# Optimization experiments

Measured on AMD Instinct MI355X. Metric: run time of the kernel, lower is better.

The kernel has to match this reference:

```python
import jax, jax.numpy as jnp
import numpy as np


def setup_inputs() -> dict:
    key = jax.random.key(0)
    k1, k2 = jax.random.split(key)
    B, N, M, D = 8, 4096, 4096, 3
    return {
        "input": jax.random.normal(k1, (B, N, D), dtype=jnp.float32),
        "target": jax.random.normal(k2, (B, M, D), dtype=jnp.float32),
    }


def reference(input, target):
    x2 = jnp.sum(input * input, axis=-1)          # [B, N]
    y2 = jnp.sum(target * target, axis=-1)        # [B, M]
    xy = jnp.einsum("bnd,bmd->bnm", input, target)  # [B, N, M]
    sqdist = x2[:, :, None] + y2[:, None, :] - 2.0 * xy
    sqdist = jnp.maximum(sqdist, 0.0)  # clamp numerical negatives
    sqdist1 = jnp.min(sqdist, axis=2)  # nearest target for each input point [B, N]
    sqdist2 = jnp.min(sqdist, axis=1)  # nearest input for each target point [B, M]
    return jnp.mean(sqdist1) + jnp.mean(sqdist2)
```

## Files before the change

### kernel.cpp

```cpp
#include <hip/hip_runtime.h>
#include <math.h>

#define BATCH 8
#define NPTS  4096
#define TPB   256
#define NCC   4
#define CHUNK (NPTS / NCC)
#define ROWS  256
#define NRC   (NPTS / ROWS)

typedef __bf16 bf16x8 __attribute__((ext_vector_type(8)));
typedef float  f32x16 __attribute__((ext_vector_type(16)));

__global__ __launch_bounds__(TPB) void chamfer_mfma_kernel(
    const float* __restrict__ input,
    const float* __restrict__ target,
    float* __restrict__ part)
{
  const int dir = blockIdx.z, b = blockIdx.y;
  const int rc = blockIdx.x & (NRC - 1);
  const int cc = blockIdx.x >> 4;

  const float* __restrict__ qp = (dir ? target : input) + (size_t)b * NPTS * 3;
  const float* __restrict__ cp = (dir ? input  : target) + (size_t)b * NPTS * 3;

  __shared__ bf16x8 sB[2][CHUNK];
  __shared__ bf16x8 sA[2][ROWS];

  {
    const int c0 = cc * CHUNK + (int)threadIdx.x * 4;
    const float4* __restrict__ cv = (const float4*)(cp + 3 * c0);
    const float4 f0 = cv[0], f1 = cv[1], f2 = cv[2];
    float xs[4] = { f0.x, f0.w, f1.z, f2.y };
    float ys[4] = { f0.y, f1.x, f1.w, f2.z };
    float zs[4] = { f0.z, f1.y, f2.x, f2.w };
    #pragma unroll
    for (int j = 0; j < 4; ++j) {
      const float mx = -2.f * xs[j], my = -2.f * ys[j], mz = -2.f * zs[j];
      const __bf16 hx = (__bf16)mx, hy = (__bf16)my, hz = (__bf16)mz;
      const __bf16 lx = (__bf16)(mx - (float)hx);
      const __bf16 ly = (__bf16)(my - (float)hy);
      const __bf16 lz = (__bf16)(mz - (float)hz);
      const float y2 = fmaf(xs[j], xs[j], fmaf(ys[j], ys[j], zs[j] * zs[j]));
      const __bf16 h2 = (__bf16)y2, l2 = (__bf16)(y2 - (float)h2);
      const __bf16 z0 = (__bf16)0.f;
      bf16x8 v0, v1;
      v0[0]=hx; v0[1]=hy; v0[2]=hz; v0[3]=lx; v0[4]=ly; v0[5]=lz; v0[6]=z0; v0[7]=z0;
      v1[0]=hx; v1[1]=hy; v1[2]=hz; v1[3]=h2; v1[4]=l2; v1[5]=z0; v1[6]=z0; v1[7]=z0;
      sB[0][threadIdx.x * 4 + j] = v0;
      sB[1][threadIdx.x * 4 + j] = v1;
    }
  }
  float qx, qy, qz;
  {
    const int r = rc * ROWS + (int)threadIdx.x;
    qx = qp[3*r]; qy = qp[3*r+1]; qz = qp[3*r+2];
    const __bf16 hx = (__bf16)qx, hy = (__bf16)qy, hz = (__bf16)qz;
    const __bf16 lx = (__bf16)(qx - (float)hx);
    const __bf16 ly = (__bf16)(qy - (float)hy);
    const __bf16 lz = (__bf16)(qz - (float)hz);
    const __bf16 z0 = (__bf16)0.f, o1 = (__bf16)1.f;
    bf16x8 v0, v1;
    v0[0]=hx; v0[1]=hy; v0[2]=hz; v0[3]=hx; v0[4]=hy; v0[5]=hz; v0[6]=z0; v0[7]=z0;
    v1[0]=lx; v1[1]=ly; v1[2]=lz; v1[3]=o1; v1[4]=o1; v1[5]=z0; v1[6]=z0; v1[7]=z0;
    sA[0][threadIdx.x] = v0;
    sA[1][threadIdx.x] = v1;
  }
  __syncthreads();

  const int lane = (int)threadIdx.x & 63;
  const int wave = (int)threadIdx.x >> 6;
  const int half = lane >> 5;
  const int l31  = lane & 31;

  const bf16x8 a0 = sA[half][wave * 64 + l31];
  const bf16x8 a1 = sA[half][wave * 64 + 32 + l31];

  float rm0[16], rm1[16];
  #pragma unroll
  for (int i = 0; i < 16; ++i) { rm0[i] = 3.4e38f; rm1[i] = 3.4e38f; }

  f32x16 zacc;
  #pragma unroll
  for (int i = 0; i < 16; ++i) zacc[i] = 0.f;

  #pragma unroll
  for (int m = 0; m < CHUNK / 32; m += 2) {
    const bf16x8 bfA = sB[half][m * 32 + l31];
    const bf16x8 bfB = sB[half][m * 32 + 32 + l31];
    const f32x16 dA0 = __builtin_amdgcn_mfma_f32_32x32x16_bf16(a0, bfA, zacc, 0, 0, 0);
    const f32x16 dA1 = __builtin_amdgcn_mfma_f32_32x32x16_bf16(a1, bfA, zacc, 0, 0, 0);
    const f32x16 dB0 = __builtin_amdgcn_mfma_f32_32x32x16_bf16(a0, bfB, zacc, 0, 0, 0);
    const f32x16 dB1 = __builtin_amdgcn_mfma_f32_32x32x16_bf16(a1, bfB, zacc, 0, 0, 0);
    #pragma unroll
    for (int i = 0; i < 16; ++i) {
      rm0[i] = fminf(fminf(dA0[i], dB0[i]), rm0[i]);
      rm1[i] = fminf(fminf(dA1[i], dB1[i]), rm1[i]);
    }
  }

  __syncthreads();
  float* __restrict__ scr = (float*)sB;
  #pragma unroll
  for (int r = 0; r < 16; ++r) {
    const int row0 = wave * 64 + (r & 3) + 8 * (r >> 2) + 4 * half;
    const int sw   = ((row0 & 7) << 2);
    scr[row0 * 32 + (l31 ^ sw)]        = rm0[r];
    scr[(row0 + 32) * 32 + (l31 ^ sw)] = rm1[r];
  }
  __syncthreads();

  const int t = (int)threadIdx.x;
  const float4* __restrict__ rp = (const float4*)(scr + t * 32);
  float mn = 3.4e38f;
  #pragma unroll
  for (int k = 0; k < 8; ++k) {
    const float4 v = rp[k ^ (t & 7)];
    mn = fminf(mn, fminf(fminf(v.x, v.y), fminf(v.z, v.w)));
  }
  const float x2 = fmaf(qx, qx, fmaf(qy, qy, qz * qz));
  part[((size_t)(dir * BATCH + b) * NCC + cc) * NPTS + rc * ROWS + t] =
      fmaxf(mn + x2, 0.f);
}

__global__ __launch_bounds__(TPB) void chamfer_reduce_kernel(
    const float* __restrict__ part, float* __restrict__ out)
{
  const int i = (blockIdx.x * TPB + (int)threadIdx.x) * 4;
  const int g = i >> 12;
  const int q = i & (NPTS - 1);

  const float* __restrict__ p = part + ((size_t)g * NCC) * NPTS + q;
  float4 mn = *(const float4*)p;
  #pragma unroll
  for (int cc = 1; cc < NCC; ++cc) {
    const float4 v = *(const float4*)(p + (size_t)cc * NPTS);
    mn.x = fminf(mn.x, v.x); mn.y = fminf(mn.y, v.y);
    mn.z = fminf(mn.z, v.z); mn.w = fminf(mn.w, v.w);
  }
  float s = mn.x + mn.y + mn.z + mn.w;
  #pragma unroll
  for (int off = 32; off > 0; off >>= 1)
    s += __shfl_down(s, off, 64);

  __shared__ float wsum[TPB / 64];
  if ((threadIdx.x & 63) == 0) wsum[threadIdx.x >> 6] = s;
  __syncthreads();
  if (threadIdx.x == 0) {
    const float v = wsum[0] + wsum[1] + wsum[2] + wsum[3];
    atomicAdd(out, v * (1.0f / (float)(BATCH * NPTS)));
  }
}

extern "C" void kernel_launch(void* const* d_in, const int* in_sizes, int n_in,
                              void* d_out, int out_size, void* d_ws, size_t ws_size,
                              hipStream_t stream) {
  const float* input  = (const float*)d_in[0];
  const float* target = (const float*)d_in[1];
  float* out  = (float*)d_out;
  float* part = (float*)d_ws;

  hipMemsetAsync(out, 0, sizeof(float), stream);

  dim3 grid1(NRC * NCC, BATCH, 2);
  chamfer_mfma_kernel<<<grid1, dim3(TPB), 0, stream>>>(input, target, part);

  dim3 grid2((2 * BATCH * NPTS) / (TPB * 4));
  chamfer_reduce_kernel<<<grid2, dim3(TPB), 0, stream>>>(part, out);
}
```

Measured before the change: 73.80 us.

## Fuse min and reduction into one kernel with full candidate set per block

Each block now stages all 4096 candidate points into shared memory instead of a quarter. It computes the full row minimum directly and reduces to the output with an atomic, which removes the partials buffer and the second reduce kernel. The grid shrinks fourfold to one block per CU with larger LDS use. This reduces latency hiding and puts the longer staging phase on the critical path.

```diff
diff --git a/kernel.cpp b/kernel.cpp
--- a/kernel.cpp
+++ b/kernel.cpp
@@ -4,51 +4,53 @@
 #define BATCH 8
 #define NPTS  4096
 #define TPB   256
-#define NCC   4
-#define CHUNK (NPTS / NCC)
 #define ROWS  256
 #define NRC   (NPTS / ROWS)
+#define CPT   (NPTS / TPB)
 
 typedef __bf16 bf16x8 __attribute__((ext_vector_type(8)));
 typedef float  f32x16 __attribute__((ext_vector_type(16)));
 
-__global__ __launch_bounds__(TPB) void chamfer_mfma_kernel(
+__global__ __launch_bounds__(TPB, 1) void chamfer_fused_kernel(
     const float* __restrict__ input,
     const float* __restrict__ target,
-    float* __restrict__ part)
+    float* __restrict__ out)
 {
-  const int dir = blockIdx.z, b = blockIdx.y;
-  const int rc = blockIdx.x & (NRC - 1);
-  const int cc = blockIdx.x >> 4;
+  const int dir = blockIdx.z, b = blockIdx.y, rc = blockIdx.x;
 
   const float* __restrict__ qp = (dir ? target : input) + (size_t)b * NPTS * 3;
   const float* __restrict__ cp = (dir ? input  : target) + (size_t)b * NPTS * 3;
 
-  __shared__ bf16x8 sB[2][CHUNK];
+  __shared__ bf16x8 sB[2][NPTS];
   __shared__ bf16x8 sA[2][ROWS];
+  __shared__ float  wsum[TPB / 64];
 
   {
-    const int c0 = cc * CHUNK + (int)threadIdx.x * 4;
+    const int c0 = (int)threadIdx.x * CPT;
     const float4* __restrict__ cv = (const float4*)(cp + 3 * c0);
-    const float4 f0 = cv[0], f1 = cv[1], f2 = cv[2];
-    float xs[4] = { f0.x, f0.w, f1.z, f2.y };
-    float ys[4] = { f0.y, f1.x, f1.w, f2.z };
-    float zs[4] = { f0.z, f1.y, f2.x, f2.w };
+    float f[3 * CPT];
     #pragma unroll
-    for (int j = 0; j < 4; ++j) {
-      const float mx = -2.f * xs[j], my = -2.f * ys[j], mz = -2.f * zs[j];
+    for (int i = 0; i < (3 * CPT) / 4; ++i) {
+      const float4 t = cv[i];
+      f[4 * i + 0] = t.x; f[4 * i + 1] = t.y;
+      f[4 * i + 2] = t.z; f[4 * i + 3] = t.w;
+    }
+    #pragma unroll
+    for (int j = 0; j < CPT; ++j) {
+      const float x = f[3 * j], y = f[3 * j + 1], z = f[3 * j + 2];
+      const float mx = -2.f * x, my = -2.f * y, mz = -2.f * z;
       const __bf16 hx = (__bf16)mx, hy = (__bf16)my, hz = (__bf16)mz;
       const __bf16 lx = (__bf16)(mx - (float)hx);
       const __bf16 ly = (__bf16)(my - (float)hy);
       const __bf16 lz = (__bf16)(mz - (float)hz);
-      const float y2 = fmaf(xs[j], xs[j], fmaf(ys[j], ys[j], zs[j] * zs[j]));
+      const float y2 = fmaf(x, x, fmaf(y, y, z * z));
       const __bf16 h2 = (__bf16)y2, l2 = (__bf16)(y2 - (float)h2);
       const __bf16 z0 = (__bf16)0.f;
       bf16x8 v0, v1;
       v0[0]=hx; v0[1]=hy; v0[2]=hz; v0[3]=lx; v0[4]=ly; v0[5]=lz; v0[6]=z0; v0[7]=z0;
       v1[0]=hx; v1[1]=hy; v1[2]=hz; v1[3]=h2; v1[4]=l2; v1[5]=z0; v1[6]=z0; v1[7]=z0;
-      sB[0][threadIdx.x * 4 + j] = v0;
-      sB[1][threadIdx.x * 4 + j] = v1;
+      sB[0][c0 + j] = v0;
+      sB[1][c0 + j] = v1;
     }
   }
   float qx, qy, qz;
@@ -84,8 +86,8 @@
   #pragma unroll
   for (int i = 0; i < 16; ++i) zacc[i] = 0.f;
 
-  #pragma unroll
-  for (int m = 0; m < CHUNK / 32; m += 2) {
+  #pragma unroll 4
+  for (int m = 0; m < NPTS / 32; m += 2) {
     const bf16x8 bfA = sB[half][m * 32 + l31];
     const bf16x8 bfB = sB[half][m * 32 + 32 + l31];
     const f32x16 dA0 = __builtin_amdgcn_mfma_f32_32x32x16_bf16(a0, bfA, zacc, 0, 0, 0);
@@ -119,31 +121,11 @@
     mn = fminf(mn, fminf(fminf(v.x, v.y), fminf(v.z, v.w)));
   }
   const float x2 = fmaf(qx, qx, fmaf(qy, qy, qz * qz));
-  part[((size_t)(dir * BATCH + b) * NCC + cc) * NPTS + rc * ROWS + t] =
-      fmaxf(mn + x2, 0.f);
-}
+  float s = fmaxf(mn + x2, 0.f);
 
-__global__ __launch_bounds__(TPB) void chamfer_reduce_kernel(
-    const float* __restrict__ part, float* __restrict__ out)
-{
-  const int i = (blockIdx.x * TPB + (int)threadIdx.x) * 4;
-  const int g = i >> 12;
-  const int q = i & (NPTS - 1);
-
-  const float* __restrict__ p = part + ((size_t)g * NCC) * NPTS + q;
-  float4 mn = *(const float4*)p;
-  #pragma unroll
-  for (int cc = 1; cc < NCC; ++cc) {
-    const float4 v = *(const float4*)(p + (size_t)cc * NPTS);
-    mn.x = fminf(mn.x, v.x); mn.y = fminf(mn.y, v.y);
-    mn.z = fminf(mn.z, v.z); mn.w = fminf(mn.w, v.w);
-  }
-  float s = mn.x + mn.y + mn.z + mn.w;
   #pragma unroll
   for (int off = 32; off > 0; off >>= 1)
     s += __shfl_down(s, off, 64);
-
-  __shared__ float wsum[TPB / 64];
   if ((threadIdx.x & 63) == 0) wsum[threadIdx.x >> 6] = s;
   __syncthreads();
   if (threadIdx.x == 0) {
@@ -157,14 +139,11 @@
                               hipStream_t stream) {
   const float* input  = (const float*)d_in[0];
   const float* target = (const float*)d_in[1];
-  float* out  = (float*)d_out;
-  float* part = (float*)d_ws;
+  float* out = (float*)d_out;
+  (void)d_ws; (void)ws_size;
 
   hipMemsetAsync(out, 0, sizeof(float), stream);
 
-  dim3 grid1(NRC * NCC, BATCH, 2);
-  chamfer_mfma_kernel<<<grid1, dim3(TPB), 0, stream>>>(input, target, part);
-
-  dim3 grid2((2 * BATCH * NPTS) / (TPB * 4));
-  chamfer_reduce_kernel<<<grid2, dim3(TPB), 0, stream>>>(part, out);
+  dim3 grid(NRC, BATCH, 2);
+  chamfer_fused_kernel<<<grid, dim3(TPB), 0, stream>>>(input, target, out);
 }
```

Result: slower. 82.14 us (+11.3%).
